# Performance work log

Measured on AMD Instinct MI355X. Metric: run time of the kernel, lower is better.

Reference implementation:

```python
import jax, jax.numpy as jnp
import numpy as np

N = 32768      # total nodes
G = 64         # graphs
NPG = 512      # nodes per graph (equal-size graphs)
K = 256        # ceil(NPG * pooling_ratio), pooling_ratio=0.5
D = 256        # input_dim
H = 256        # hidden_dim
FD = 3 * H     # fusion dim
C = 10         # num_classes
E = 262144     # edges
EPS = 1e-5     # BatchNorm eps


def setup_inputs() -> dict:
    key = jax.random.key(0)
    ks = jax.random.split(key, 20)
    w = lambda k, s: jax.random.normal(k, s, jnp.float32) * 0.05
    inp = {
        'x': jax.random.normal(ks[0], (N, D), jnp.float32),
        'edge_index': jax.random.randint(ks[1], (2, E), 0, N, jnp.int64),
        'batch': (jnp.arange(N, dtype=jnp.int64) // NPG),
        'w_s1': w(ks[2], (D, H)), 'b_s1': jnp.zeros((H,), jnp.float32),
        'w_s21': w(ks[3], (D, H)), 'b_s21': jnp.zeros((H,), jnp.float32),
        'w_s22': w(ks[4], (H, H)), 'b_s22': jnp.zeros((H,), jnp.float32),
        'w_raw': w(ks[5], (D, H)), 'b_raw': jnp.zeros((H,), jnp.float32),
        'w_pos': w(ks[6], (FD, 1)), 'b_pos': jnp.zeros((1,), jnp.float32),
        'w_neg': w(ks[7], (FD, 1)), 'b_neg': jnp.zeros((1,), jnp.float32),
        'w_pool': w(ks[8], (FD, FD)), 'b_pool': jnp.zeros((FD,), jnp.float32),
        'w1': w(ks[9], (2 * FD, 256)), 'b1': jnp.zeros((256,), jnp.float32),
        'g1': jnp.ones((256,), jnp.float32), 'be1': jnp.zeros((256,), jnp.float32),
        'w2': w(ks[10], (256, 256)), 'b2': jnp.zeros((256,), jnp.float32),
        'g2': jnp.ones((256,), jnp.float32), 'be2': jnp.zeros((256,), jnp.float32),
        'w3': w(ks[11], (256, 256)), 'b3': jnp.zeros((256,), jnp.float32),
        'g3': jnp.ones((256,), jnp.float32), 'be3': jnp.zeros((256,), jnp.float32),
        'w4': w(ks[12], (256, C)), 'b4': jnp.zeros((C,), jnp.float32),
    }
    return inp


def _gcn(x, W, b, src, dst, dinv):
    # PyG GCNConv: linear, then sym-normalized aggregation with self-loops
    h = x @ W
    norm = dinv[src] * dinv[dst]
    agg = jax.ops.segment_sum(h[src] * norm[:, None], dst, num_segments=N)
    agg = agg + h * (dinv * dinv)[:, None]  # self-loop contribution
    return agg + b


def _bn(z, g, b):
    m = z.mean(0)
    v = z.var(0)  # biased, as torch BN training-mode normalization
    return (z - m) * jax.lax.rsqrt(v + EPS) * g + b


def _mlp(z, w1, b1, g1, be1, w2, b2, g2, be2, w3, b3, g3, be3, w4, b4):
    z = jax.nn.relu(_bn(z @ w1 + b1, g1, be1))  # dropout=identity (eval)
    idt = z
    o = jax.nn.relu(_bn(z @ w2 + b2, g2, be2))
    z = o + idt
    idt = z
    o = jax.nn.relu(_bn(z @ w3 + b3, g3, be3))
    z = o + idt
    return z @ w4 + b4


def _topk_mask(scores):
    # equal-size graphs -> per-graph top-k via one batched lax.top_k
    sg = scores.reshape(G, NPG)
    _, idx = jax.lax.top_k(sg, K)
    mask = jnp.zeros((G, NPG), bool).at[jnp.arange(G)[:, None], idx].set(True)
    return mask.reshape(-1)


def _readout(xt, mask):
    m = mask[:, None]
    xs = jnp.where(m, xt, 0.0).reshape(G, NPG, FD)
    mean_pool = xs.sum(1) / K
    mx = jnp.where(m, xt, -jnp.inf).reshape(G, NPG, FD).max(1)
    return jnp.concatenate([mean_pool, mx], axis=1)


def reference(x, edge_index, batch, w_s1, b_s1, w_s21, b_s21, w_s22, b_s22,
              w_raw, b_raw, w_pos, b_pos, w_neg, b_neg, w_pool, b_pool,
              w1, b1, g1, be1, w2, b2, g2, be2, w3, b3, g3, be3, w4, b4):
    src, dst = edge_index[0], edge_index[1]
    deg = jax.ops.segment_sum(jnp.ones_like(src, jnp.float32), dst, num_segments=N) + 1.0
    dinv = jax.lax.rsqrt(deg)
    lrelu = lambda z: jax.nn.leaky_relu(z, 0.01)

    h_s1 = lrelu(_gcn(x, w_s1, b_s1, src, dst, dinv))
    h_s2 = lrelu(_gcn(lrelu(_gcn(x, w_s21, b_s21, src, dst, dinv)), w_s22, b_s22, src, dst, dinv))
    h_raw = x @ w_raw + b_raw
    h_final = jnp.concatenate([h_s1, h_s2, h_raw], axis=1)  # [N, FD]

    score_pos = jax.nn.sigmoid(_gcn(h_final, w_pos, b_pos, src, dst, dinv)).reshape(-1)
    score_neg = jax.nn.sigmoid(_gcn(h_final, w_neg, b_neg, src, dst, dinv)).reshape(-1)

    xt = jax.nn.sigmoid(h_final @ w_pool + b_pool)  # pool_transform for all nodes; mask selects
    mask_pos = _topk_mask(score_pos)
    mask_neg = _topk_mask(score_neg)

    mlp = lambda e: _mlp(e, w1, b1, g1, be1, w2, b2, g2, be2, w3, b3, g3, be3, w4, b4)
    logits_pos = mlp(_readout(xt, mask_pos))
    probs_pos = jax.nn.softmax(logits_pos, axis=1)
    logits_neg = mlp(_readout(xt, mask_neg))
    probs_neg = jax.nn.softmax(logits_neg, axis=1)
    return (logits_pos, probs_pos, probs_neg, score_pos, score_neg, batch)
```

## Files before the change

kernel.cpp:

```cpp
#include <hip/hip_runtime.h>
#include <hip/hip_bf16.h>

#define N_NODES 32768
#define NGRAPH  64
#define NPG     512
#define TOPK    256
#define HID     256
#define FDIM    768
#define NEDGE   262144
#define NCLS    10
#define BN_EPS  1e-5f

#define IN_BF16 0
#define OUT_BF16 0

typedef __attribute__((ext_vector_type(8))) short short8;
typedef __attribute__((ext_vector_type(4))) float f32x4;

__device__ __forceinline__ float bf2f(unsigned short u) {
    return __uint_as_float(((unsigned)u) << 16);
}
__device__ __forceinline__ unsigned short f2bf(float f) {
    unsigned x = __float_as_uint(f);
    unsigned r = (x + 0x7fffu + ((x >> 16) & 1u)) >> 16;
    return (unsigned short)r;
}
__device__ __forceinline__ float in_ld(const void* p, size_t i) {
#if IN_BF16
    return bf2f(((const unsigned short*)p)[i]);
#else
    return ((const float*)p)[i];
#endif
}
__device__ __forceinline__ void st_out(void* o, size_t i, float v) {
#if OUT_BF16
    ((unsigned short*)o)[i] = f2bf(v);
#else
    ((float*)o)[i] = v;
#endif
}

__device__ __forceinline__ void async_cp16(const unsigned short* g, unsigned short* l) {
    __builtin_amdgcn_global_load_lds(
        (const __attribute__((address_space(1))) unsigned int*)g,
        (__attribute__((address_space(3))) unsigned int*)l, 16, 0, 0);
}

__device__ __forceinline__ void tile_swizzle(int& bm, int& bn) {
    int nx = gridDim.x;
    int L = blockIdx.y * nx + blockIdx.x;
    int xcd = L & 7;
    int j = L >> 3;
    bm = ((j / nx) * 8 + xcd) * 128;
    bn = (j % nx) * 128;
}

__global__ __launch_bounds__(256) void cvt_all_kernel(const float* __restrict__ x,
                                                      const float* __restrict__ w_s1,
                                                      const float* __restrict__ w_s21,
                                                      const float* __restrict__ w_s22,
                                                      const float* __restrict__ w_raw,
                                                      const float* __restrict__ w_pool,
                                                      unsigned short* __restrict__ xbf,
                                                      unsigned short* __restrict__ wcat2,
                                                      unsigned short* __restrict__ wb_s22,
                                                      unsigned short* __restrict__ wb_raw,
                                                      unsigned short* __restrict__ wb_pool) {
    int id = blockIdx.x;
    if (id < 4096) {
        size_t base = (size_t)id * 2048 + threadIdx.x * 8;
        float4 a = *(const float4*)(x + base);
        float4 b = *(const float4*)(x + base + 4);
        unsigned short o[8] = { f2bf(a.x), f2bf(a.y), f2bf(a.z), f2bf(a.w),
                                f2bf(b.x), f2bf(b.y), f2bf(b.z), f2bf(b.w) };
        *(uint4*)(xbf + base) = *(uint4*)o;
        return;
    }
    __shared__ unsigned short tile[32][33];
    const float* src;
    unsigned short* dst;
    int K, N, t;
    if (id < 4160)      { src = w_s1;  dst = wcat2;                     K = 256; N = 256; t = id - 4096; }
    else if (id < 4224) { src = w_s21; dst = wcat2 + (size_t)256 * 256; K = 256; N = 256; t = id - 4160; }
    else if (id < 4288) { src = w_s22; dst = wb_s22;                    K = 256; N = 256; t = id - 4224; }
    else if (id < 4352) { src = w_raw; dst = wb_raw;                    K = 256; N = 256; t = id - 4288; }
    else                { src = w_pool; dst = wb_pool;                  K = 768; N = 768; t = id - 4352; }
    int tiles_x = K >> 5;
    int bk = (t % tiles_x) * 32, bn = (t / tiles_x) * 32;
    int tx = threadIdx.x & 31, ty = threadIdx.x >> 5;
#pragma unroll
    for (int i = 0; i < 32; i += 8)
        tile[ty + i][tx] = f2bf(src[(size_t)(bk + ty + i) * N + bn + tx]);
    __syncthreads();
#pragma unroll
    for (int i = 0; i < 32; i += 8)
        dst[(size_t)(bn + ty + i) * K + bk + tx] = tile[tx][ty + i];
}

__global__ __launch_bounds__(256) void detect_kernel(const int* __restrict__ eb, int* __restrict__ flag) {
    int i = blockIdx.x * 256 + threadIdx.x;
    int v = eb[2 * (size_t)i + 1];
    unsigned long long b = __ballot(v != 0);
    if ((threadIdx.x & 63) == 0 && b)
        atomicAdd(flag, (int)__popcll(b));
}

__global__ __launch_bounds__(256) void hist_kernel(const int* __restrict__ eb, const int* __restrict__ flag,
                                                   int* __restrict__ deg) {
    int e = blockIdx.x * 256 + threadIdx.x;
    int st = (*flag == 0) ? 2 : 1;
    unsigned d = ((const unsigned*)eb)[(size_t)(NEDGE + e) * st] & (N_NODES - 1);
    atomicAdd(&deg[d], 1);
}

__global__ __launch_bounds__(1024) void scan_kernel(const int* __restrict__ cnt, int* __restrict__ rowptr,
                                                    int* __restrict__ cursor, float* __restrict__ dinv) {
    __shared__ int part[1024];
    int t = threadIdx.x;
    int base = t * 32;
    int loc[32];
    int s = 0;
#pragma unroll
    for (int i = 0; i < 32; i++) { loc[i] = cnt[base + i]; s += loc[i]; }
    part[t] = s;
    __syncthreads();
    for (int off = 1; off < 1024; off <<= 1) {
        int v = (t >= off) ? part[t - off] : 0;
        __syncthreads();
        part[t] += v;
        __syncthreads();
    }
    int run = (t == 0) ? 0 : part[t - 1];
#pragma unroll
    for (int i = 0; i < 32; i++) {
        rowptr[base + i] = run;
        cursor[base + i] = run;
        dinv[base + i] = rsqrtf((float)loc[i] + 1.0f);
        run += loc[i];
    }
    if (t == 1023) rowptr[N_NODES] = run;
}

__global__ __launch_bounds__(256) void scatter_kernel(const int* __restrict__ eb, const int* __restrict__ flag,
                                                      int* __restrict__ cursor, int* __restrict__ srcs) {
    int e = blockIdx.x * 256 + threadIdx.x;
    int st = (*flag == 0) ? 2 : 1;
    unsigned s = ((const unsigned*)eb)[(size_t)e * st] & (N_NODES - 1);
    unsigned d = ((const unsigned*)eb)[(size_t)(NEDGE + e) * st] & (N_NODES - 1);
    int p = atomicAdd(&cursor[d], 1);
    srcs[p] = (int)s;
}

#define GEMM_BODY(K_)                                                           \
    __shared__ unsigned short As[128 * 64];                                     \
    __shared__ unsigned short Bs[128 * 64];                                     \
    const int tid = threadIdx.x;                                                \
    const int wave = tid >> 6;                                                  \
    const int lane = tid & 63;                                                  \
    const int wm = (wave >> 1) * 64;                                            \
    const int wn = (wave & 1) * 64;                                             \
    const int l15 = lane & 15;                                                  \
    const int q = lane >> 4;                                                    \
    f32x4 acc[4][4] = {};                                                       \
    const int srow = lane >> 3;                                                 \
    const int schunk = lane & 7;                                                \
    const int gc = schunk ^ srow;                                               \
    const unsigned short* gaA = A + (size_t)(bm + wave * 8 + srow) * (K_) + gc * 8;  \
    const unsigned short* gbB = WT + (size_t)(bn + wave * 8 + srow) * (K_) + gc * 8; \
    const size_t K32 = (size_t)(K_) * 32;                                       \
    unsigned short* const la0 = &As[(wave * 8) * 64];                           \
    unsigned short* const lb0 = &Bs[(wave * 8) * 64];                           \
    for (int k0 = 0; k0 < (K_); k0 += 64) {                                     \
        __syncthreads();                                                        \
        _Pragma("unroll")                                                       \
        for (int t = 0; t < 4; t++) {                                           \
            async_cp16(gaA + t * K32 + k0, la0 + t * 32 * 64);                  \
            async_cp16(gbB + t * K32 + k0, lb0 + t * 32 * 64);                  \
        }                                                                       \
        __syncthreads();                                                        \
        _Pragma("unroll")                                                       \
        for (int h = 0; h < 2; h++) {                                           \
            short8 af[4], bfv[4];                                               \
            int p = (h * 4 + q) ^ (l15 & 7);                                    \
            _Pragma("unroll")                                                   \
            for (int t = 0; t < 4; t++) {                                       \
                int m = wm + t * 16 + l15;                                      \
                int n = wn + t * 16 + l15;                                      \
                af[t] = *(const short8*)&As[m * 64 + p * 8];                    \
                bfv[t] = *(const short8*)&Bs[n * 64 + p * 8];                   \
            }                                                                   \
            _Pragma("unroll")                                                   \
            for (int tm = 0; tm < 4; tm++)                                      \
                _Pragma("unroll")                                               \
                for (int tn = 0; tn < 4; tn++)                                  \
                    acc[tm][tn] = __builtin_amdgcn_mfma_f32_16x16x32_bf16(af[tm], bfv[tn], acc[tm][tn], 0, 0, 0); \
        }                                                                       \
    }

__global__ __launch_bounds__(256) void gemm_kernel(const unsigned short* __restrict__ A,
                                                   const unsigned short* __restrict__ WT,
                                                   const float* __restrict__ bias,
                                                   unsigned short* __restrict__ C,
                                                   int K, int ldC, int colOff, int epi) {
    int bm, bn;
    tile_swizzle(bm, bn);
    GEMM_BODY(K)
#pragma unroll
    for (int tm = 0; tm < 4; tm++) {
        int row = bm + wm + tm * 16 + q * 4;
#pragma unroll
        for (int tn = 0; tn < 4; tn++) {
            int col = bn + wn + tn * 16 + l15;
            float bv = bias ? bias[col] : 0.0f;
#pragma unroll
            for (int r = 0; r < 4; r++) {
                float v = acc[tm][tn][r] + bv;
                if (epi == 1) v = 1.0f / (1.0f + __expf(-v));
                else if (epi == 2) v = v > 0.f ? v : 0.01f * v;
                C[(size_t)(row + r) * ldC + colOff + col] = f2bf(v);
            }
        }
    }
}

__global__ __launch_bounds__(256) void gemmA6_kernel(const unsigned short* __restrict__ Xa,
                                                     const unsigned short* __restrict__ wcat2,
                                                     const unsigned short* __restrict__ xbf,
                                                     const unsigned short* __restrict__ wb_raw,
                                                     const float* __restrict__ b_s1,
                                                     const float* __restrict__ b_s21,
                                                     const float* __restrict__ b_raw,
                                                     unsigned short* __restrict__ hfin,
                                                     unsigned short* __restrict__ t1) {
    const int nx = 6;
    int L = blockIdx.y * nx + blockIdx.x;
    int xcd = L & 7, j = L >> 3;
    int bm = ((j / nx) * 8 + xcd) * 128;
    int bnt = j % nx;
    int sub = (bnt < 4) ? 0 : 1;
    const unsigned short* A = sub ? xbf : Xa;
    const unsigned short* WT = sub ? wb_raw : wcat2;
    int bn = sub ? (bnt - 4) * 128 : bnt * 128;
    GEMM_BODY(256)
#pragma unroll
    for (int tm = 0; tm < 4; tm++) {
        int row = bm + wm + tm * 16 + q * 4;
#pragma unroll
        for (int tn = 0; tn < 4; tn++) {
            int col = bn + wn + tn * 16 + l15;
            if (sub == 0) {
                if (col < 256) {
                    float bv = b_s1[col];
#pragma unroll
                    for (int r = 0; r < 4; r++) {
                        float v = acc[tm][tn][r] + bv;
                        v = v > 0.f ? v : 0.01f * v;
                        hfin[(size_t)(row + r) * 768 + col] = f2bf(v);
                    }
                } else {
                    float bv = b_s21[col - 256];
#pragma unroll
                    for (int r = 0; r < 4; r++) {
                        float v = acc[tm][tn][r] + bv;
                        v = v > 0.f ? v : 0.01f * v;
                        t1[(size_t)(row + r) * 256 + (col - 256)] = f2bf(v);
                    }
                }
            } else {
                float bv = b_raw[col];
#pragma unroll
                for (int r = 0; r < 4; r++)
                    hfin[(size_t)(row + r) * 768 + 512 + col] = f2bf(acc[tm][tn][r] + bv);
            }
        }
    }
}

__global__ __launch_bounds__(256) void lin_agg_kernel(const unsigned short* __restrict__ h,
                                                      const int* __restrict__ rowptr, const int* __restrict__ srcs,
                                                      const float* __restrict__ dinv,
                                                      unsigned short* __restrict__ out) {
    int wave = threadIdx.x >> 6, lane = threadIdx.x & 63;
    int v = blockIdx.x * 4 + wave;
    int f0 = lane * 4;
    float a0 = 0.f, a1 = 0.f, a2 = 0.f, a3 = 0.f;
    int s = rowptr[v], e = rowptr[v + 1];
    for (int i = s; i < e; i++) {
        int u = srcs[i] & (N_NODES - 1);
        float du = dinv[u];
        uint2 hv = *(const uint2*)(h + (size_t)u * 256 + f0);
        a0 += bf2f((unsigned short)(hv.x & 0xffff)) * du;
        a1 += bf2f((unsigned short)(hv.x >> 16)) * du;
        a2 += bf2f((unsigned short)(hv.y & 0xffff)) * du;
        a3 += bf2f((unsigned short)(hv.y >> 16)) * du;
    }
    float dv = dinv[v], dv2 = dv * dv;
    uint2 sv = *(const uint2*)(h + (size_t)v * 256 + f0);
    float r0 = dv * a0 + bf2f((unsigned short)(sv.x & 0xffff)) * dv2;
    float r1 = dv * a1 + bf2f((unsigned short)(sv.x >> 16)) * dv2;
    float r2 = dv * a2 + bf2f((unsigned short)(sv.y & 0xffff)) * dv2;
    float r3 = dv * a3 + bf2f((unsigned short)(sv.y >> 16)) * dv2;
    uint2 ov = make_uint2(((unsigned)f2bf(r1) << 16) | f2bf(r0), ((unsigned)f2bf(r3) << 16) | f2bf(r2));
    *(uint2*)(out + (size_t)v * 256 + f0) = ov;
}

__global__ __launch_bounds__(256) void score_mv_kernel(const unsigned short* __restrict__ hf,
                                                       const void* __restrict__ wp, const void* __restrict__ wn,
                                                       float* __restrict__ svp, float* __restrict__ svn) {
    int wave = threadIdx.x >> 6, lane = threadIdx.x & 63;
    int v = blockIdx.x * 4 + wave;
    float sp = 0.f, sn = 0.f;
#pragma unroll
    for (int i = 0; i < 3; i++) {
        int k = i * 256 + lane * 4;
        uint2 hv = *(const uint2*)(hf + (size_t)v * 768 + k);
        float x0 = bf2f((unsigned short)(hv.x & 0xffff));
        float x1 = bf2f((unsigned short)(hv.x >> 16));
        float x2 = bf2f((unsigned short)(hv.y & 0xffff));
        float x3 = bf2f((unsigned short)(hv.y >> 16));
        sp += x0 * in_ld(wp, k) + x1 * in_ld(wp, k + 1) + x2 * in_ld(wp, k + 2) + x3 * in_ld(wp, k + 3);
        sn += x0 * in_ld(wn, k) + x1 * in_ld(wn, k + 1) + x2 * in_ld(wn, k + 2) + x3 * in_ld(wn, k + 3);
    }
    for (int off = 32; off >= 1; off >>= 1) {
        sp += __shfl_down(sp, off, 64);
        sn += __shfl_down(sn, off, 64);
    }
    if (lane == 0) { svp[v] = sp; svn[v] = sn; }
}

__global__ __launch_bounds__(512) void score_topk_kernel(const float* __restrict__ svp, const float* __restrict__ svn,
                                                         const int* __restrict__ rowptr, const int* __restrict__ srcs,
                                                         const float* __restrict__ dinv,
                                                         const void* __restrict__ bp, const void* __restrict__ bn_,
                                                         unsigned char* __restrict__ maskp,
                                                         unsigned char* __restrict__ maskn,
                                                         void* __restrict__ dout) {
    __shared__ float sp[512], sn[512];
    int g = blockIdx.x, i = threadIdx.x;
    int v = g * 512 + i;
    float ap = 0.f, an = 0.f;
    int s = rowptr[v], e = rowptr[v + 1];
    for (int k = s; k < e; k++) {
        int u = srcs[k] & (N_NODES - 1);
        float du = dinv[u];
        ap += svp[u] * du;
        an += svn[u] * du;
    }
    float dv = dinv[v], dv2 = dv * dv;
    float zp = dv * ap + svp[v] * dv2 + in_ld(bp, 0);
    float zn = dv * an + svn[v] * dv2 + in_ld(bn_, 0);
    float pp = 1.0f / (1.0f + __expf(-zp));
    float pn = 1.0f / (1.0f + __expf(-zn));
    st_out(dout, 1920 + (size_t)v, pp);
    st_out(dout, 1920 + (size_t)N_NODES + v, pn);
    st_out(dout, 1920 + 2 * (size_t)N_NODES + v, (float)g);
    sp[i] = pp; sn[i] = pn;
    __syncthreads();
    int cp = 0, cn = 0;
    for (int j = 0; j < 512; j++) {
        float op = sp[j], on = sn[j];
        cp += (int)((op > pp) || ((op == pp) && (j < i)));
        cn += (int)((on > pn) || ((on == pn) && (j < i)));
    }
    maskp[v] = (cp < TOPK) ? 1 : 0;
    maskn[v] = (cn < TOPK) ? 1 : 0;
}

__global__ __launch_bounds__(256) void readout2_kernel(const unsigned short* __restrict__ xt,
                                                       const unsigned char* __restrict__ maskp,
                                                       const unsigned char* __restrict__ maskn,
                                                       float* __restrict__ eout) {
    int g = blockIdx.x;
    int c = blockIdx.y;
    int wv = threadIdx.x >> 6, lane = threadIdx.x & 63;
    int f = c * 64 + lane;
    __shared__ unsigned char mp[512], mn[512];
    __shared__ float red[4][64][4];
    for (int i = threadIdx.x; i < 512; i += 256) {
        mp[i] = maskp[(size_t)g * 512 + i];
        mn[i] = maskn[(size_t)g * 512 + i];
    }
    __syncthreads();
    float sp = 0.f, sn = 0.f, xp = -INFINITY, xn = -INFINITY;
    const unsigned short* base = xt + ((size_t)g * 512 + wv * 128) * 768 + f;
    for (int v = 0; v < 128; v++) {
        unsigned char bp = mp[wv * 128 + v], bn_ = mn[wv * 128 + v];
        if (!(bp | bn_)) continue;
        float x = bf2f(base[(size_t)v * 768]);
        if (bp) { sp += x; xp = fmaxf(xp, x); }
        if (bn_) { sn += x; xn = fmaxf(xn, x); }
    }
    red[wv][lane][0] = sp; red[wv][lane][1] = xp;
    red[wv][lane][2] = sn; red[wv][lane][3] = xn;
    __syncthreads();
    if (wv == 0) {
#pragma unroll
        for (int w = 1; w < 4; w++) {
            sp += red[w][lane][0]; xp = fmaxf(xp, red[w][lane][1]);
            sn += red[w][lane][2]; xn = fmaxf(xn, red[w][lane][3]);
        }
        float* erp = eout + (size_t)g * 1536;
        float* ern = eout + (size_t)(64 + g) * 1536;
        erp[f] = sp * (1.0f / TOPK);
        erp[768 + f] = xp;
        ern[f] = sn * (1.0f / TOPK);
        ern[768 + f] = xn;
    }
}

__global__ __launch_bounds__(256) void mlp_gemm2_kernel(const float* __restrict__ in,
                                                        const float* __restrict__ W,
                                                        const float* __restrict__ b,
                                                        float* __restrict__ out, int K) {
    __shared__ float row[1536];
    __shared__ float red[4][64];
    int r = blockIdx.x, cg = blockIdx.y;
    int wv = threadIdx.x >> 6, lane = threadIdx.x & 63;
    int c = cg * 64 + lane;
    for (int k = threadIdx.x; k < K; k += 256) row[k] = in[(size_t)r * K + k];
    __syncthreads();
    int kpw = K >> 2;
    const float* wp = W + (size_t)(wv * kpw) * 256 + c;
    const float* rp = row + wv * kpw;
    float acc = 0.f;
#pragma unroll 4
    for (int k = 0; k < kpw; k++)
        acc += rp[k] * wp[(size_t)k * 256];
    red[wv][lane] = acc;
    __syncthreads();
    if (wv == 0) {
        float v = red[0][lane] + red[1][lane] + red[2][lane] + red[3][lane] + b[c];
        out[(size_t)r * 256 + c] = v;
    }
}

__global__ __launch_bounds__(64) void bn_kernel(const float* __restrict__ z, const void* __restrict__ gamma,
                                                const void* __restrict__ beta, const float* __restrict__ res,
                                                float* __restrict__ out) {
    int f = blockIdx.x & 255, g = blockIdx.x >> 8, r = threadIdx.x;
    size_t idx = (size_t)(g * 64 + r) * 256 + f;
    float x = z[idx];
    float s = x, sq = x * x;
    for (int off = 1; off < 64; off <<= 1) {
        s += __shfl_xor(s, off, 64);
        sq += __shfl_xor(sq, off, 64);
    }
    float m = s * (1.0f / 64.0f);
    float var = sq * (1.0f / 64.0f) - m * m;
    float y = (x - m) * rsqrtf(var + BN_EPS) * in_ld(gamma, f) + in_ld(beta, f);
    y = fmaxf(y, 0.0f);
    if (res) y += res[idx];
    out[idx] = y;
}

__global__ __launch_bounds__(64) void head_kernel(const float* __restrict__ act, const void* __restrict__ w4,
                                                  const void* __restrict__ b4, void* __restrict__ dout) {
    __shared__ float l[NCLS];
    int r = blockIdx.x, t = threadIdx.x;
    if (t < NCLS) {
        float acc = in_ld(b4, t);
        for (int k = 0; k < 256; k++)
            acc += act[(size_t)r * 256 + k] * in_ld(w4, (size_t)k * NCLS + t);
        l[t] = acc;
    }
    __syncthreads();
    if (t == 0) {
        float mx = -1e30f;
        for (int c = 0; c < NCLS; c++) mx = fmaxf(mx, l[c]);
        float ex[NCLS], sum = 0.f;
        for (int c = 0; c < NCLS; c++) { ex[c] = __expf(l[c] - mx); sum += ex[c]; }
        float inv = 1.0f / sum;
        int g = r >> 6, rr = r & 63;
        if (g == 0) {
            for (int c = 0; c < NCLS; c++) st_out(dout, (size_t)rr * NCLS + c, l[c]);
            for (int c = 0; c < NCLS; c++) st_out(dout, 640 + (size_t)rr * NCLS + c, ex[c] * inv);
        } else {
            for (int c = 0; c < NCLS; c++) st_out(dout, 1280 + (size_t)rr * NCLS + c, ex[c] * inv);
        }
    }
}

extern "C" void kernel_launch(void* const* d_in, const int* in_sizes, int n_in,
                              void* d_out, int out_size, void* d_ws, size_t ws_size,
                              hipStream_t stream) {
    (void)in_sizes; (void)n_in; (void)out_size; (void)ws_size;

    const float* x = (const float*)d_in[0];
    const int* eb = (const int*)d_in[1];
    const float* w_s1 = (const float*)d_in[3];
    const float* b_s1 = (const float*)d_in[4];
    const float* w_s21 = (const float*)d_in[5];
    const float* b_s21 = (const float*)d_in[6];
    const float* w_s22 = (const float*)d_in[7];
    const float* b_s22 = (const float*)d_in[8];
    const float* w_raw = (const float*)d_in[9];
    const float* b_raw = (const float*)d_in[10];
    const void* w_pos = d_in[11];
    const void* b_pos = d_in[12];
    const void* w_neg = d_in[13];
    const void* b_neg = d_in[14];
    const float* w_pool = (const float*)d_in[15];
    const float* b_pool = (const float*)d_in[16];
    const float* w1 = (const float*)d_in[17];  const float* b1 = (const float*)d_in[18];
    const void* g1 = d_in[19];  const void* be1 = d_in[20];
    const float* w2 = (const float*)d_in[21];  const float* b2 = (const float*)d_in[22];
    const void* g2 = d_in[23];  const void* be2 = d_in[24];
    const float* w3 = (const float*)d_in[25];  const float* b3 = (const float*)d_in[26];
    const void* g3 = d_in[27];  const void* be3 = d_in[28];
    const void* w4 = d_in[29];  const void* b4 = d_in[30];

    char* ws = (char*)d_ws;
    size_t off = 0;
    auto alloc = [&](size_t b) -> void* {
        void* p = ws + off;
        off += (b + 255) & ~(size_t)255;
        return p;
    };
    int* flag = (int*)alloc(256);
    int* deg = (int*)alloc((size_t)N_NODES * 4);
    float* dinv = (float*)alloc((size_t)N_NODES * 4);
    int* rowptr = (int*)alloc((size_t)(N_NODES + 1) * 4);
    int* cursor = (int*)alloc((size_t)N_NODES * 4);
    int* srcs = (int*)alloc((size_t)NEDGE * 4);
    unsigned short* xbf = (unsigned short*)alloc((size_t)N_NODES * 256 * 2);
    unsigned short* wcat2 = (unsigned short*)alloc((size_t)512 * 256 * 2);
    unsigned short* wb_s22 = (unsigned short*)alloc((size_t)256 * 256 * 2);
    unsigned short* wb_raw = (unsigned short*)alloc((size_t)256 * 256 * 2);
    unsigned short* wb_pool = (unsigned short*)alloc((size_t)768 * 768 * 2);
    unsigned short* Xa = (unsigned short*)alloc((size_t)N_NODES * 256 * 2);
    unsigned short* t1 = (unsigned short*)alloc((size_t)N_NODES * 256 * 2);
    unsigned short* t1a = (unsigned short*)alloc((size_t)N_NODES * 256 * 2);
    unsigned short* hfin = (unsigned short*)alloc((size_t)N_NODES * 768 * 2);
    unsigned short* xt = (unsigned short*)alloc((size_t)N_NODES * 768 * 2);
    float* svp = (float*)alloc((size_t)N_NODES * 4);
    float* svn = (float*)alloc((size_t)N_NODES * 4);
    unsigned char* maskp = (unsigned char*)alloc(N_NODES);
    unsigned char* maskn = (unsigned char*)alloc(N_NODES);
    float* ebuf = (float*)alloc((size_t)128 * 1536 * 4);
    float* zb = (float*)alloc((size_t)128 * 256 * 4);
    float* act1 = (float*)alloc((size_t)128 * 256 * 4);
    float* act2 = (float*)alloc((size_t)128 * 256 * 4);
    float* act3 = (float*)alloc((size_t)128 * 256 * 4);

    hipMemsetAsync(flag, 0, 256 + (size_t)N_NODES * 4, stream);

    detect_kernel<<<NEDGE / 256, 256, 0, stream>>>(eb, flag);
    hist_kernel<<<NEDGE / 256, 256, 0, stream>>>(eb, flag, deg);
    scan_kernel<<<1, 1024, 0, stream>>>(deg, rowptr, cursor, dinv);
    scatter_kernel<<<NEDGE / 256, 256, 0, stream>>>(eb, flag, cursor, srcs);

    cvt_all_kernel<<<4928, 256, 0, stream>>>(x, w_s1, w_s21, w_s22, w_raw, w_pool,
                                             xbf, wcat2, wb_s22, wb_raw, wb_pool);

    dim3 gA6(6, N_NODES / 128);
    dim3 gA1(2, N_NODES / 128);
    dim3 gP(6, N_NODES / 128);

    lin_agg_kernel<<<N_NODES / 4, 256, 0, stream>>>(xbf, rowptr, srcs, dinv, Xa);
    gemmA6_kernel<<<gA6, 256, 0, stream>>>(Xa, wcat2, xbf, wb_raw, b_s1, b_s21, b_raw, hfin, t1);
    lin_agg_kernel<<<N_NODES / 4, 256, 0, stream>>>(t1, rowptr, srcs, dinv, t1a);
    gemm_kernel<<<gA1, 256, 0, stream>>>(t1a, wb_s22, b_s22, hfin, 256, 768, 256, 2);
    gemm_kernel<<<gP, 256, 0, stream>>>(hfin, wb_pool, b_pool, xt, 768, 768, 0, 1);
    score_mv_kernel<<<N_NODES / 4, 256, 0, stream>>>(hfin, w_pos, w_neg, svp, svn);
    score_topk_kernel<<<NGRAPH, 512, 0, stream>>>(svp, svn, rowptr, srcs, dinv, b_pos, b_neg,
                                                  maskp, maskn, d_out);
    {
        dim3 gR(NGRAPH, FDIM / 64);
        readout2_kernel<<<gR, 256, 0, stream>>>(xt, maskp, maskn, ebuf);
    }
    {
        dim3 gM(128, 4);
        mlp_gemm2_kernel<<<gM, 256, 0, stream>>>(ebuf, w1, b1, zb, 1536);
        bn_kernel<<<512, 64, 0, stream>>>(zb, g1, be1, nullptr, act1);
        mlp_gemm2_kernel<<<gM, 256, 0, stream>>>(act1, w2, b2, zb, 256);
        bn_kernel<<<512, 64, 0, stream>>>(zb, g2, be2, act1, act2);
        mlp_gemm2_kernel<<<gM, 256, 0, stream>>>(act2, w3, b3, zb, 256);
        bn_kernel<<<512, 64, 0, stream>>>(zb, g3, be3, act2, act3);
    }
    head_kernel<<<128, 64, 0, stream>>>(act3, w4, b4, d_out);
}
```

Baseline: 578.9 us.

## Fuse MLP linear layers with BatchNorm into tiled per-group kernels

```diff
diff --git a/kernel.cpp b/kernel.cpp
--- a/kernel.cpp
+++ b/kernel.cpp
@@ -408,49 +408,68 @@
     }
 }
 
-__global__ __launch_bounds__(256) void mlp_gemm2_kernel(const float* __restrict__ in,
+__global__ __launch_bounds__(256) void mlp_layer_kernel(const float* __restrict__ in,
                                                         const float* __restrict__ W,
                                                         const float* __restrict__ b,
+                                                        const float* __restrict__ gamma,
+                                                        const float* __restrict__ beta,
+                                                        const float* __restrict__ res,
                                                         float* __restrict__ out, int K) {
-    __shared__ float row[1536];
-    __shared__ float red[4][64];
-    int r = blockIdx.x, cg = blockIdx.y;
-    int wv = threadIdx.x >> 6, lane = threadIdx.x & 63;
-    int c = cg * 64 + lane;
-    for (int k = threadIdx.x; k < K; k += 256) row[k] = in[(size_t)r * K + k];
-    __syncthreads();
-    int kpw = K >> 2;
-    const float* wp = W + (size_t)(wv * kpw) * 256 + c;
-    const float* rp = row + wv * kpw;
-    float acc = 0.f;
-#pragma unroll 4
-    for (int k = 0; k < kpw; k++)
-        acc += rp[k] * wp[(size_t)k * 256];
-    red[wv][lane] = acc;
-    __syncthreads();
-    if (wv == 0) {
-        float v = red[0][lane] + red[1][lane] + red[2][lane] + red[3][lane] + b[c];
-        out[(size_t)r * 256 + c] = v;
-    }
-}
-
-__global__ __launch_bounds__(64) void bn_kernel(const float* __restrict__ z, const void* __restrict__ gamma,
-                                                const void* __restrict__ beta, const float* __restrict__ res,
-                                                float* __restrict__ out) {
-    int f = blockIdx.x & 255, g = blockIdx.x >> 8, r = threadIdx.x;
-    size_t idx = (size_t)(g * 64 + r) * 256 + f;
-    float x = z[idx];
-    float s = x, sq = x * x;
-    for (int off = 1; off < 64; off <<= 1) {
-        s += __shfl_xor(s, off, 64);
-        sq += __shfl_xor(sq, off, 64);
-    }
-    float m = s * (1.0f / 64.0f);
-    float var = sq * (1.0f / 64.0f) - m * m;
-    float y = (x - m) * rsqrtf(var + BN_EPS) * in_ld(gamma, f) + in_ld(beta, f);
-    y = fmaxf(y, 0.0f);
-    if (res) y += res[idx];
-    out[idx] = y;
+    __shared__ float inS[64][129];
+    __shared__ float wS[128][17];
+    __shared__ float red[16][16][2];
+    __shared__ float mv[16][2];
+    int g = blockIdx.x, cg = blockIdx.y;
+    int t = threadIdx.x;
+    int c16 = t & 15, rb = t >> 4;
+    int col = cg * 16 + c16;
+    float acc[4] = {0.f, 0.f, 0.f, 0.f};
+    for (int k0 = 0; k0 < K; k0 += 128) {
+        __syncthreads();
+        for (int idx = t; idx < 64 * 128; idx += 256) {
+            int r = idx >> 7, kk = idx & 127;
+            inS[r][kk] = in[(size_t)(g * 64 + r) * K + k0 + kk];
+        }
+        for (int idx = t; idx < 128 * 16; idx += 256) {
+            int k = idx >> 4, c = idx & 15;
+            wS[k][c] = W[(size_t)(k0 + k) * 256 + cg * 16 + c];
+        }
+        __syncthreads();
+        for (int k = 0; k < 128; k++) {
+            float w = wS[k][c16];
+            acc[0] += inS[rb * 4 + 0][k] * w;
+            acc[1] += inS[rb * 4 + 1][k] * w;
+            acc[2] += inS[rb * 4 + 2][k] * w;
+            acc[3] += inS[rb * 4 + 3][k] * w;
+        }
+    }
+    float bv = b[col];
+#pragma unroll
+    for (int j = 0; j < 4; j++) acc[j] += bv;
+    float s = acc[0] + acc[1] + acc[2] + acc[3];
+    float sq = acc[0] * acc[0] + acc[1] * acc[1] + acc[2] * acc[2] + acc[3] * acc[3];
+    red[rb][c16][0] = s;
+    red[rb][c16][1] = sq;
+    __syncthreads();
+    if (rb == 0) {
+        float S = 0.f, Q = 0.f;
+#pragma unroll
+        for (int i = 0; i < 16; i++) { S += red[i][c16][0]; Q += red[i][c16][1]; }
+        float m = S * (1.0f / 64.0f);
+        mv[c16][0] = m;
+        mv[c16][1] = rsqrtf(Q * (1.0f / 64.0f) - m * m + BN_EPS);
+    }
+    __syncthreads();
+    float m = mv[c16][0], inv = mv[c16][1];
+    float ga = gamma[col], be = beta[col];
+#pragma unroll
+    for (int j = 0; j < 4; j++) {
+        int row = g * 64 + rb * 4 + j;
+        float y = (acc[j] - m) * inv * ga + be;
+        y = fmaxf(y, 0.0f);
+        if (res) y += res[(size_t)row * 256 + col];
+        out[(size_t)row * 256 + col] = y;
+    }
 }
 
 __global__ __launch_bounds__(64) void head_kernel(const float* __restrict__ act, const void* __restrict__ w4,
@@ -502,11 +521,11 @@
     const float* w_pool = (const float*)d_in[15];
     const float* b_pool = (const float*)d_in[16];
     const float* w1 = (const float*)d_in[17];  const float* b1 = (const float*)d_in[18];
-    const void* g1 = d_in[19];  const void* be1 = d_in[20];
+    const float* g1 = (const float*)d_in[19];  const float* be1 = (const float*)d_in[20];
     const float* w2 = (const float*)d_in[21];  const float* b2 = (const float*)d_in[22];
-    const void* g2 = d_in[23];  const void* be2 = d_in[24];
+    const float* g2 = (const float*)d_in[23];  const float* be2 = (const float*)d_in[24];
     const float* w3 = (const float*)d_in[25];  const float* b3 = (const float*)d_in[26];
-    const void* g3 = d_in[27];  const void* be3 = d_in[28];
+    const float* g3 = (const float*)d_in[27];  const float* be3 = (const float*)d_in[28];
     const void* w4 = d_in[29];  const void* b4 = d_in[30];
 
     char* ws = (char*)d_ws;
@@ -537,7 +556,6 @@
     unsigned char* maskp = (unsigned char*)alloc(N_NODES);
     unsigned char* maskn = (unsigned char*)alloc(N_NODES);
     float* ebuf = (float*)alloc((size_t)128 * 1536 * 4);
-    float* zb = (float*)alloc((size_t)128 * 256 * 4);
     float* act1 = (float*)alloc((size_t)128 * 256 * 4);
     float* act2 = (float*)alloc((size_t)128 * 256 * 4);
     float* act3 = (float*)alloc((size_t)128 * 256 * 4);
@@ -569,13 +587,10 @@
         readout2_kernel<<<gR, 256, 0, stream>>>(xt, maskp, maskn, ebuf);
     }
     {
-        dim3 gM(128, 4);
-        mlp_gemm2_kernel<<<gM, 256, 0, stream>>>(ebuf, w1, b1, zb, 1536);
-        bn_kernel<<<512, 64, 0, stream>>>(zb, g1, be1, nullptr, act1);
-        mlp_gemm2_kernel<<<gM, 256, 0, stream>>>(act1, w2, b2, zb, 256);
-        bn_kernel<<<512, 64, 0, stream>>>(zb, g2, be2, act1, act2);
-        mlp_gemm2_kernel<<<gM, 256, 0, stream>>>(act2, w3, b3, zb, 256);
-        bn_kernel<<<512, 64, 0, stream>>>(zb, g3, be3, act2, act3);
+        dim3 gL(2, 16);
+        mlp_layer_kernel<<<gL, 256, 0, stream>>>(ebuf, w1, b1, g1, be1, nullptr, act1, 1536);
+        mlp_layer_kernel<<<gL, 256, 0, stream>>>(act1, w2, b2, g2, be2, act1, act2, 256);
+        mlp_layer_kernel<<<gL, 256, 0, stream>>>(act2, w3, b3, g3, be3, act2, act3, 256);
     }
     head_kernel<<<128, 64, 0, stream>>>(act3, w4, b4, d_out);
 }
```

After: 645.1 us. 1.11x slower.
